# Performance work log

Hardware: AMD Instinct MI355X
Metric: run time of the kernel (lower is better)

## Reference

```python
import jax, jax.numpy as jnp
import numpy as np

N_NODES = 100000


def gcn_conv(x, edge_index, W, b, n_nodes):
    """PyG GCNConv: h = x @ W; add self-loops; symmetric deg norm; sum-aggregate; + bias."""
    src, dst = edge_index[0], edge_index[1]
    loop = jnp.arange(n_nodes, dtype=src.dtype)
    src = jnp.concatenate([src, loop])  # [E + N]
    dst = jnp.concatenate([dst, loop])
    w = jnp.ones(src.shape[0], dtype=x.dtype)  # edge_weight=None -> ones
    deg = jax.ops.segment_sum(w, dst, num_segments=n_nodes)  # in-degree incl. self-loop
    dinv = jnp.where(deg > 0, jax.lax.rsqrt(deg), 0.0).astype(x.dtype)
    norm = dinv[src] * w * dinv[dst]  # [E + N]
    h = x @ W  # [N, d_out] transform first (PyG order)
    msgs = norm[:, None] * h[src]  # [E + N, d_out] gathered, normalized messages
    out = jax.ops.segment_sum(msgs, dst, num_segments=n_nodes)
    return out + b


def setup_inputs() -> dict:
    key = jax.random.key(0)
    k1, k2, k3, k4 = jax.random.split(key, 4)
    d_in, d_hid, d_out = 128, 128, 64
    E = 3200000
    x = jax.random.normal(k1, (N_NODES, d_in), dtype=jnp.float32)
    edge_index = jax.random.randint(k2, (2, E), 0, N_NODES, dtype=jnp.int64)
    W1 = jax.random.normal(k3, (d_in, d_hid), dtype=jnp.float32) / np.sqrt(d_in)
    b1 = jnp.zeros((d_hid,), dtype=jnp.float32)
    W2 = jax.random.normal(k4, (d_hid, d_out), dtype=jnp.float32) / np.sqrt(d_hid)
    b2 = jnp.zeros((d_out,), dtype=jnp.float32)
    return {"x": x, "edge_index": edge_index, "W1": W1, "b1": b1, "W2": W2, "b2": b2}


def reference(x, edge_index, W1, b1, W2, b2):
    h = gcn_conv(x, edge_index, W1, b1, N_NODES)
    h = jax.nn.relu(h)
    out = gcn_conv(h, edge_index, W2, b2, N_NODES)
    return out
```

## Files before the change

kernel.cpp:

```cpp
#include <hip/hip_runtime.h>


#define N_NODES 100000
#define NBLK2 256
#define NBUCK2 782
#define NCH 13
#define NKEY (NBUCK2 * NCH)

#define FPS  1048576.0f
#define INVS 9.5367431640625e-7f

typedef __attribute__((ext_vector_type(8))) short short8;
typedef __attribute__((ext_vector_type(4))) float f32x4;

__device__ __forceinline__ unsigned short f2bf(float f) {
    union { float f; unsigned u; } c; c.f = f;
    unsigned r = (c.u + 0x7fffu + ((c.u >> 16) & 1u)) >> 16;
    return (unsigned short)r;
}
__device__ __forceinline__ float2 bfpair(unsigned u) {
    union { float f; unsigned u; } a, b;
    a.u = u << 16; b.u = u & 0xffff0000u;
    return make_float2(a.f, b.f);
}
__device__ __forceinline__ unsigned packbf(float a, float b) {
    return (unsigned)f2bf(a) | ((unsigned)f2bf(b) << 16);
}
__device__ __forceinline__ int fp20(float v) {
    return __float2int_rn(v * FPS);
}

__global__ void detect64_k(const unsigned long long* __restrict__ ei, int* __restrict__ flag) {
    unsigned long long v = ei[threadIdx.x & 63];
    unsigned long long bad = __ballot(v >= (1ULL << 32));
    if (threadIdx.x == 0) *flag = (bad == 0ULL) ? 1 : 0;
}

__device__ __forceinline__ int edge_at(const void* ei, int is64, long long idx) {
    if (is64) return (int)((const long long*)ei)[idx];
    return ((const int*)ei)[idx];
}

__global__ __launch_bounds__(256) void count1_k(const void* __restrict__ ei,
                                                const int* __restrict__ flag,
                                                int* __restrict__ bhist, int E) {
    __shared__ int lh[NKEY];
    int t = threadIdx.x;
    for (int i = t; i < NKEY; i += 256) lh[i] = 0;
    __syncthreads();
    int is64 = *flag;
    int C = (E + NBLK2 - 1) / NBLK2;
    int lo = blockIdx.x * C;
    int hi = lo + C; if (hi > E) hi = E;
    for (int e = lo + t; e < hi; e += 256) {
        int s = edge_at(ei, is64, e);
        int d = edge_at(ei, is64, (long long)E + e);
        if ((unsigned)d >= (unsigned)N_NODES) continue;
        if ((unsigned)s >= (unsigned)N_NODES) s = 0;
        atomicAdd(&lh[(d >> 7) * NCH + (s >> 13)], 1);
    }
    __syncthreads();
    int* dst = bhist + (size_t)blockIdx.x * NKEY;
    for (int i = t; i < NKEY; i += 256) dst[i] = lh[i];
}

__global__ void colsum_k(const int* __restrict__ bhist, int* __restrict__ colsum) {
    int k = blockIdx.x * 256 + threadIdx.x;
    if (k >= NKEY) return;
    int s = 0;
#pragma unroll 4
    for (int b = 0; b < NBLK2; ++b) s += bhist[(size_t)b * NKEY + k];
    colsum[k] = s;
}

__global__ void scan1_k(const int* __restrict__ cnt, int* __restrict__ partial,
                        int* __restrict__ bsum, int n) {
    __shared__ int sm[256];
    int t = threadIdx.x;
    int base = blockIdx.x * 1024 + t * 4;
    int v[4]; int loc = 0;
#pragma unroll
    for (int j = 0; j < 4; ++j) { v[j] = (base + j < n) ? cnt[base + j] : 0; loc += v[j]; }
    sm[t] = loc; __syncthreads();
    for (int off = 1; off < 256; off <<= 1) {
        int x = (t >= off) ? sm[t - off] : 0;
        __syncthreads();
        sm[t] += x;
        __syncthreads();
    }
    int incl = sm[t];
    int run = incl - loc;
    if (t == 255) bsum[blockIdx.x] = incl;
#pragma unroll
    for (int j = 0; j < 4; ++j) {
        if (base + j < n) partial[base + j] = run;
        run += v[j];
    }
}

__global__ void scan2_k(int* __restrict__ bsum, int nb) {
    __shared__ int sm[256];
    int t = threadIdx.x;
    int v[16]; int loc = 0;
#pragma unroll
    for (int i = 0; i < 16; ++i) {
        int idx = t * 16 + i;
        v[i] = (idx < nb) ? bsum[idx] : 0;
        loc += v[i];
    }
    sm[t] = loc; __syncthreads();
    for (int off = 1; off < 256; off <<= 1) {
        int x = (t >= off) ? sm[t - off] : 0;
        __syncthreads();
        sm[t] += x;
        __syncthreads();
    }
    int run = sm[t] - loc;
#pragma unroll
    for (int i = 0; i < 16; ++i) {
        int idx = t * 16 + i;
        if (idx < nb) bsum[idx] = run;
        run += v[i];
    }
}

__global__ void scanadd_k(const int* __restrict__ bsum, int* __restrict__ arr,
                          const int* __restrict__ raw, int* __restrict__ tot, int n) {
    int base = blockIdx.x * 1024 + threadIdx.x * 4;
    int add = bsum[blockIdx.x];
#pragma unroll
    for (int j = 0; j < 4; ++j) {
        int i = base + j;
        if (i < n) {
            int v = arr[i] + add;
            arr[i] = v;
            if (i == n - 1) *tot = v + raw[i];
        }
    }
}

__global__ void colprefix_k(const int* __restrict__ bhist, const int* __restrict__ keybase,
                            int* __restrict__ bbase) {
    int k = blockIdx.x * 256 + threadIdx.x;
    if (k >= NKEY) return;
    int run = keybase[k];
#pragma unroll 8
    for (int b = 0; b < NBLK2; ++b) {
        size_t i = (size_t)b * NKEY + k;
        int c = bhist[i];
        bbase[i] = run;
        run += c;
    }
}

__global__ void dinv_k(const int* __restrict__ cnt, float* __restrict__ dinv, int n) {
    int i = blockIdx.x * 256 + threadIdx.x;
    if (i < n) dinv[i] = rsqrtf((float)(cnt[i] + 1));
}

__global__ __launch_bounds__(256) void write1_k(const void* __restrict__ ei,
                                                const int* __restrict__ flag,
                                                const int* __restrict__ bbase,
                                                unsigned* __restrict__ pairs, int E) {
    __shared__ int lofs[NKEY];
    int t = threadIdx.x;
    const int* src0 = bbase + (size_t)blockIdx.x * NKEY;
    for (int i = t; i < NKEY; i += 256) lofs[i] = src0[i];
    __syncthreads();
    int is64 = *flag;
    int C = (E + NBLK2 - 1) / NBLK2;
    int lo = blockIdx.x * C;
    int hi = lo + C; if (hi > E) hi = E;
    for (int e = lo + t; e < hi; e += 256) {
        int s = edge_at(ei, is64, e);
        int d = edge_at(ei, is64, (long long)E + e);
        if ((unsigned)d >= (unsigned)N_NODES) continue;
        if ((unsigned)s >= (unsigned)N_NODES) s = 0;
        int key = (d >> 7) * NCH + (s >> 13);
        int p = atomicAdd(&lofs[key], 1);
        pairs[p] = (unsigned)s | ((unsigned)(d & 127) << 17);
    }
}

__global__ __launch_bounds__(256) void degree_k(const unsigned* __restrict__ pairs,
                                                const int* __restrict__ keybase,
                                                const int* __restrict__ tot,
                                                int* __restrict__ cnt, int Nn) {
    __shared__ int lh[128];
    int b = blockIdx.x;
    int t = threadIdx.x;
    if (t < 128) lh[t] = 0;
    __syncthreads();
    int lo = keybase[b * NCH];
    int hi = (b == NBUCK2 - 1) ? *tot : keybase[(b + 1) * NCH];
    for (int i = lo + t; i < hi; i += 256) {
        unsigned p = __builtin_nontemporal_load(pairs + i);
        atomicAdd(&lh[p >> 17], 1);
    }
    __syncthreads();
    int n0 = b << 7;
    if (t < 128 && n0 + t < Nn) cnt[n0 + t] = lh[t];
}

__global__ void prep_w_k(const float* __restrict__ W1, const float* __restrict__ W2,
                         unsigned short* __restrict__ w1bf, unsigned short* __restrict__ w2bf) {
    int i = blockIdx.x * 256 + threadIdx.x;
    if (i < 128 * 128) { int k = i >> 7, f = i & 127; w1bf[f * 128 + k] = f2bf(W1[i]); }
    if (i < 128 * 64)  { int k = i >> 6, f = i & 63;  w2bf[f * 128 + k] = f2bf(W2[i]); }
}

__global__ __launch_bounds__(256) void gemm1_k(const float* __restrict__ x,
                                               const unsigned short* __restrict__ w1bf,
                                               const float* __restrict__ dinv,
                                               unsigned* __restrict__ h1, int Nn) {
    __shared__ __align__(16) unsigned short sA[128][136];
    __shared__ __align__(16) unsigned short sB[64][136];
    int tid = threadIdx.x;
    int n0g = blockIdx.x * 64;
    {
        const uint4* src = (const uint4*)w1bf;
#pragma unroll
        for (int l = 0; l < 8; ++l) {
            int idx = tid + l * 256;
            int f = idx >> 4, kq = idx & 15;
            *(uint4*)&sA[f][kq * 8] = src[idx];
        }
    }
    {
        int n = tid >> 2, kq = tid & 3;
        int gn = n0g + n; if (gn >= Nn) gn = Nn - 1;
        const float4* xr = (const float4*)(x + (size_t)gn * 128 + kq * 32);
        unsigned short* dst = &sB[n][kq * 32];
#pragma unroll
        for (int i = 0; i < 8; ++i) {
            float4 v = xr[i];
            dst[i * 4 + 0] = f2bf(v.x); dst[i * 4 + 1] = f2bf(v.y);
            dst[i * 4 + 2] = f2bf(v.z); dst[i * 4 + 3] = f2bf(v.w);
        }
    }
    __syncthreads();
    int wave = tid >> 6, lane = tid & 63;
    int quad = lane >> 4, l16 = lane & 15;
    f32x4 z = {0.f, 0.f, 0.f, 0.f};
    f32x4 acc[8];
#pragma unroll
    for (int t = 0; t < 8; ++t) acc[t] = z;
#pragma unroll
    for (int kk = 0; kk < 4; ++kk) {
        int kb = kk * 32 + quad * 8;
        short8 a = *(const short8*)&sB[wave * 16 + l16][kb];
#pragma unroll
        for (int ft = 0; ft < 8; ++ft) {
            short8 b = *(const short8*)&sA[ft * 16 + l16][kb];
            acc[ft] = __builtin_amdgcn_mfma_f32_16x16x32_bf16(a, b, acc[ft], 0, 0, 0);
        }
    }
    float dv[4];
#pragma unroll
    for (int r = 0; r < 4; ++r) {
        int gn = n0g + wave * 16 + quad * 4 + r;
        if (gn >= Nn) gn = Nn - 1;
        dv[r] = dinv[gn];
    }
    __syncthreads();
    unsigned short (*sC)[136] = sA;
#pragma unroll
    for (int ft = 0; ft < 8; ++ft)
#pragma unroll
        for (int r = 0; r < 4; ++r)
            sC[wave * 16 + quad * 4 + r][ft * 16 + l16] = f2bf(dv[r] * acc[ft][r]);
    __syncthreads();
#pragma unroll
    for (int l = 0; l < 4; ++l) {
        int idx = tid + l * 256;
        int row = idx >> 4, g = idx & 15;
        int gn = n0g + row;
        if (gn < Nn) {
            ushort4 A = *(ushort4*)&sC[row][g * 4];
            ushort4 B = *(ushort4*)&sC[row][g * 4 + 64];
            uint4 o;
            o.x = (unsigned)A.x | ((unsigned)B.x << 16);
            o.y = (unsigned)A.y | ((unsigned)B.y << 16);
            o.z = (unsigned)A.z | ((unsigned)B.z << 16);
            o.w = (unsigned)A.w | ((unsigned)B.w << 16);
            *(uint4*)&h1[(size_t)gn * 64 + g * 4] = o;
        }
    }
}

__global__ __launch_bounds__(256) void gemm2_k(const unsigned* __restrict__ hr,
                                               const unsigned short* __restrict__ w2bf,
                                               const float* __restrict__ dinv,
                                               unsigned* __restrict__ h2, int Nn) {
    __shared__ __align__(16) unsigned short sA[64][136];
    __shared__ __align__(16) unsigned short sB[64][136];
    int tid = threadIdx.x;
    int n0g = blockIdx.x * 64;
    {
        const uint4* src = (const uint4*)w2bf;
#pragma unroll
        for (int l = 0; l < 4; ++l) {
            int idx = tid + l * 256;
            int f = idx >> 4, kq = idx & 15;
            *(uint4*)&sA[f][kq * 8] = src[idx];
        }
    }
    {
        const uint4* src = (const uint4*)hr;
#pragma unroll
        for (int l = 0; l < 4; ++l) {
            int idx = tid + l * 256;
            int row = idx >> 4, q = idx & 15;
            int gn = n0g + row; if (gn >= Nn) gn = Nn - 1;
            *(uint4*)&sB[row][q * 8] = src[(size_t)gn * 16 + q];
        }
    }
    __syncthreads();
    int wave = tid >> 6, lane = tid & 63;
    int quad = lane >> 4, l16 = lane & 15;
    f32x4 z = {0.f, 0.f, 0.f, 0.f};
    f32x4 acc[4];
#pragma unroll
    for (int t = 0; t < 4; ++t) acc[t] = z;
#pragma unroll
    for (int kk = 0; kk < 4; ++kk) {
        int kb = kk * 32 + quad * 8;
        short8 a = *(const short8*)&sB[wave * 16 + l16][kb];
#pragma unroll
        for (int ft = 0; ft < 4; ++ft) {
            short8 b = *(const short8*)&sA[ft * 16 + l16][kb];
            acc[ft] = __builtin_amdgcn_mfma_f32_16x16x32_bf16(a, b, acc[ft], 0, 0, 0);
        }
    }
    float dv[4];
#pragma unroll
    for (int r = 0; r < 4; ++r) {
        int gn = n0g + wave * 16 + quad * 4 + r;
        if (gn >= Nn) gn = Nn - 1;
        dv[r] = dinv[gn];
    }
    __syncthreads();
    unsigned short (*sC)[136] = sA;
#pragma unroll
    for (int ft = 0; ft < 4; ++ft)
#pragma unroll
        for (int r = 0; r < 4; ++r)
            sC[wave * 16 + quad * 4 + r][ft * 16 + l16] = f2bf(dv[r] * acc[ft][r]);
    __syncthreads();
#pragma unroll
    for (int l = 0; l < 2; ++l) {
        int idx = tid + l * 256;
        int row = idx >> 3, g = idx & 7;
        int gn = n0g + row;
        if (gn < Nn) {
            ushort4 A = *(ushort4*)&sC[row][g * 4];
            ushort4 B = *(ushort4*)&sC[row][g * 4 + 32];
            uint4 o;
            o.x = (unsigned)A.x | ((unsigned)B.x << 16);
            o.y = (unsigned)A.y | ((unsigned)B.y << 16);
            o.z = (unsigned)A.z | ((unsigned)B.z << 16);
            o.w = (unsigned)A.w | ((unsigned)B.w << 16);
            *(uint4*)&h2[(size_t)gn * 32 + g * 4] = o;
        }
    }
}

__global__ __launch_bounds__(512) void agg1_k(const unsigned* __restrict__ h,
                                              const unsigned* __restrict__ pairs,
                                              const int* __restrict__ keybase,
                                              const int* __restrict__ tot,
                                              const float* __restrict__ dinv,
                                              const float* __restrict__ bias,
                                              unsigned* __restrict__ out, int Nn) {
    extern __shared__ int iacc[];
    int tid = threadIdx.x, lane = tid & 63, wave = tid >> 6;
    int b = blockIdx.x, n0 = b << 7;
    for (int i = tid; i < 128 * 64; i += 512) {
        int row = i >> 6, q = i & 63;
        unsigned u = (n0 + row < Nn) ? h[(size_t)(n0 + row) * 64 + q] : 0u;
        float2 v = bfpair(u);
        iacc[row * 128 + q] = fp20(v.x);
        iacc[row * 128 + 64 + q] = fp20(v.y);
    }
    __syncthreads();
    int lo = keybase[b * NCH];
    int hi = (b == NBUCK2 - 1) ? *tot : keybase[(b + 1) * NCH];
    for (int base = lo + wave * 64; base < hi; base += 512) {
        int idx = base + lane;
        unsigned pv = pairs[(idx < hi) ? idx : (hi - 1)];
        int m = hi - base; if (m > 64) m = 64;
        int j = 0;
        for (; j + 4 <= m; j += 4) {
            unsigned p0 = __shfl(pv, j),     p1 = __shfl(pv, j + 1);
            unsigned p2 = __shfl(pv, j + 2), p3 = __shfl(pv, j + 3);
            unsigned u0 = h[((p0 & 0x1FFFFu) << 6) + lane];
            unsigned u1 = h[((p1 & 0x1FFFFu) << 6) + lane];
            unsigned u2 = h[((p2 & 0x1FFFFu) << 6) + lane];
            unsigned u3 = h[((p3 & 0x1FFFFu) << 6) + lane];
            float2 v0 = bfpair(u0); int* a0 = &iacc[((p0 >> 17) << 7) + lane];
            atomicAdd(a0, fp20(v0.x)); atomicAdd(a0 + 64, fp20(v0.y));
            float2 v1 = bfpair(u1); int* a1 = &iacc[((p1 >> 17) << 7) + lane];
            atomicAdd(a1, fp20(v1.x)); atomicAdd(a1 + 64, fp20(v1.y));
            float2 v2 = bfpair(u2); int* a2 = &iacc[((p2 >> 17) << 7) + lane];
            atomicAdd(a2, fp20(v2.x)); atomicAdd(a2 + 64, fp20(v2.y));
            float2 v3 = bfpair(u3); int* a3 = &iacc[((p3 >> 17) << 7) + lane];
            atomicAdd(a3, fp20(v3.x)); atomicAdd(a3 + 64, fp20(v3.y));
        }
        for (; j < m; ++j) {
            unsigned p = __shfl(pv, j);
            unsigned u = h[((p & 0x1FFFFu) << 6) + lane];
            float2 v = bfpair(u);
            int* a = &iacc[((p >> 17) << 7) + lane];
            atomicAdd(a, fp20(v.x)); atomicAdd(a + 64, fp20(v.y));
        }
    }
    __syncthreads();
    int nn = Nn - n0; if (nn > 128) nn = 128;
    for (int i = tid; i < nn * 64; i += 512) {
        int row = i >> 6, q = i & 63;
        float di = dinv[n0 + row];
        float sx = (float)iacc[row * 128 + 2 * q] * INVS;
        float sy = (float)iacc[row * 128 + 2 * q + 1] * INVS;
        float r0 = fmaxf(fmaf(di, sx, bias[2 * q]), 0.f);
        float r1 = fmaxf(fmaf(di, sy, bias[2 * q + 1]), 0.f);
        out[(size_t)(n0 + row) * 64 + q] = packbf(r0, r1);
    }
}

__global__ __launch_bounds__(512) void agg2_k(const unsigned* __restrict__ h,
                                              const unsigned* __restrict__ pairs,
                                              const int* __restrict__ keybase,
                                              const int* __restrict__ tot,
                                              const float* __restrict__ dinv,
                                              const float* __restrict__ bias,
                                              float* __restrict__ out, int Nn) {
    __shared__ int iacc[128 * 64];
    int tid = threadIdx.x, lane = tid & 63, wave = tid >> 6;
    int half = lane >> 5, fl = lane & 31;
    int b = blockIdx.x, n0 = b << 7;
    for (int i = tid; i < 128 * 32; i += 512) {
        int row = i >> 5, q = i & 31;
        unsigned u = (n0 + row < Nn) ? h[(size_t)(n0 + row) * 32 + q] : 0u;
        float2 v = bfpair(u);
        iacc[row * 64 + q] = fp20(v.x);
        iacc[row * 64 + 32 + q] = fp20(v.y);
    }
    __syncthreads();
    int lo = keybase[b * NCH];
    int hi = (b == NBUCK2 - 1) ? *tot : keybase[(b + 1) * NCH];
    for (int base = lo + wave * 64; base < hi; base += 512) {
        int idx = base + lane;
        unsigned pv = pairs[(idx < hi) ? idx : (hi - 1)];
        int m = hi - base; if (m > 64) m = 64;
        int j = 0;
        for (; j + 8 <= m; j += 8) {
            unsigned p0 = __shfl(pv, j + half);
            unsigned p1 = __shfl(pv, j + 2 + half);
            unsigned p2 = __shfl(pv, j + 4 + half);
            unsigned p3 = __shfl(pv, j + 6 + half);
            unsigned u0 = h[((p0 & 0x1FFFFu) << 5) + fl];
            unsigned u1 = h[((p1 & 0x1FFFFu) << 5) + fl];
            unsigned u2 = h[((p2 & 0x1FFFFu) << 5) + fl];
            unsigned u3 = h[((p3 & 0x1FFFFu) << 5) + fl];
            float2 v0 = bfpair(u0); int* a0 = &iacc[((p0 >> 17) << 6) + fl];
            atomicAdd(a0, fp20(v0.x)); atomicAdd(a0 + 32, fp20(v0.y));
            float2 v1 = bfpair(u1); int* a1 = &iacc[((p1 >> 17) << 6) + fl];
            atomicAdd(a1, fp20(v1.x)); atomicAdd(a1 + 32, fp20(v1.y));
            float2 v2 = bfpair(u2); int* a2 = &iacc[((p2 >> 17) << 6) + fl];
            atomicAdd(a2, fp20(v2.x)); atomicAdd(a2 + 32, fp20(v2.y));
            float2 v3 = bfpair(u3); int* a3 = &iacc[((p3 >> 17) << 6) + fl];
            atomicAdd(a3, fp20(v3.x)); atomicAdd(a3 + 32, fp20(v3.y));
        }
        for (; j < m; j += 2) {
            int q = j + half;
            unsigned p = __shfl(pv, (q < m) ? q : j);
            if (q < m) {
                unsigned u = h[((p & 0x1FFFFu) << 5) + fl];
                float2 v = bfpair(u);
                int* a = &iacc[((p >> 17) << 6) + fl];
                atomicAdd(a, fp20(v.x)); atomicAdd(a + 32, fp20(v.y));
            }
        }
    }
    __syncthreads();
    int nn = Nn - n0; if (nn > 128) nn = 128;
    for (int i = tid; i < nn * 64; i += 512) {
        int row = i >> 6, f = i & 63;
        float di = dinv[n0 + row];
        float s = (float)iacc[row * 64 + f] * INVS;
        out[(size_t)(n0 + row) * 64 + f] = fmaf(di, s, bias[f]);
    }
}

extern "C" void kernel_launch(void* const* d_in, const int* in_sizes, int n_in,
                              void* d_out, int out_size, void* d_ws, size_t ws_size,
                              hipStream_t stream) {
    const float* x  = (const float*)d_in[0];
    const void*  ei = d_in[1];
    const float* W1 = (const float*)d_in[2];
    const float* b1 = (const float*)d_in[3];
    const float* W2 = (const float*)d_in[4];
    const float* b2 = (const float*)d_in[5];

    const int N = N_NODES;
    const int E = in_sizes[1] / 2;

    char* w = (char*)d_ws;
    size_t off = 0;
    auto take = [&](size_t bytes) {
        void* p = w + off;
        off = (off + bytes + 255) & ~(size_t)255;
        return p;
    };
    int*   flag    = (int*)take(2 * sizeof(int));
    int*   tot     = flag + 1;
    int*   cnt     = (int*)take((size_t)N * 4);
    int*   bsumB   = (int*)take(4096 * 4);
    int*   colsum  = (int*)take((size_t)NKEY * 4);
    int*   keybase = (int*)take((size_t)NKEY * 4);
    float* dinv    = (float*)take((size_t)N * 4);
    unsigned* pairs = (unsigned*)take((size_t)E * 4);
    unsigned short* w1bf = (unsigned short*)take(128 * 128 * 2);
    unsigned short* w2bf = (unsigned short*)take(64 * 128 * 2);
    unsigned* hr   = (unsigned*)take((size_t)N * 64 * 4);
    unsigned* h2   = (unsigned*)take((size_t)N * 32 * 4);
    (void)ws_size; (void)n_in; (void)out_size;

    int* bhist = (int*)hr;
    int* bbase = (int*)h2;

    unsigned* h1 = (unsigned*)d_out;

    const int nscanK = (NKEY + 1023) / 1024;
    const int ngridK = (NKEY + 255) / 256;

    detect64_k<<<1, 64, 0, stream>>>((const unsigned long long*)ei, flag);
    count1_k<<<NBLK2, 256, 0, stream>>>(ei, flag, bhist, E);
    colsum_k<<<ngridK, 256, 0, stream>>>(bhist, colsum);
    scan1_k<<<nscanK, 256, 0, stream>>>(colsum, keybase, bsumB, NKEY);
    scan2_k<<<1, 256, 0, stream>>>(bsumB, nscanK);
    scanadd_k<<<nscanK, 256, 0, stream>>>(bsumB, keybase, colsum, tot, NKEY);
    colprefix_k<<<ngridK, 256, 0, stream>>>(bhist, keybase, bbase);
    write1_k<<<NBLK2, 256, 0, stream>>>(ei, flag, bbase, pairs, E);
    degree_k<<<NBUCK2, 256, 0, stream>>>(pairs, keybase, tot, cnt, N);
    dinv_k<<<(N + 255) / 256, 256, 0, stream>>>(cnt, dinv, N);
    prep_w_k<<<64, 256, 0, stream>>>(W1, W2, w1bf, w2bf);

    gemm1_k<<<(N + 63) / 64, 256, 0, stream>>>(x, w1bf, dinv, h1, N);
    agg1_k<<<NBUCK2, 512, 128 * 128 * 4, stream>>>(h1, pairs, keybase, tot, dinv, b1, hr, N);
    gemm2_k<<<(N + 63) / 64, 256, 0, stream>>>(hr, w2bf, dinv, h2, N);
    agg2_k<<<NBUCK2, 512, 0, stream>>>(h2, pairs, keybase, tot, dinv, b2, (float*)d_out, N);
}
```

Baseline: 484.6 us.

## Store GEMM outputs as int16 fixed-point and widen aggregation blocks to 1024 threads

```diff
diff --git a/kernel.cpp b/kernel.cpp
--- a/kernel.cpp
+++ b/kernel.cpp
@@ -7,8 +7,8 @@
 #define NCH 13
 #define NKEY (NBUCK2 * NCH)
 
-#define FPS  1048576.0f
-#define INVS 9.5367431640625e-7f
+#define QS   8192.0f
+#define IQS  1.220703125e-4f
 
 typedef __attribute__((ext_vector_type(8))) short short8;
 typedef __attribute__((ext_vector_type(4))) float f32x4;
@@ -18,16 +18,13 @@
     unsigned r = (c.u + 0x7fffu + ((c.u >> 16) & 1u)) >> 16;
     return (unsigned short)r;
 }
-__device__ __forceinline__ float2 bfpair(unsigned u) {
-    union { float f; unsigned u; } a, b;
-    a.u = u << 16; b.u = u & 0xffff0000u;
-    return make_float2(a.f, b.f);
-}
 __device__ __forceinline__ unsigned packbf(float a, float b) {
     return (unsigned)f2bf(a) | ((unsigned)f2bf(b) << 16);
 }
-__device__ __forceinline__ int fp20(float v) {
-    return __float2int_rn(v * FPS);
+__device__ __forceinline__ unsigned short q13(float v) {
+    int i = __float2int_rn(v * QS);
+    i = i < -32767 ? -32767 : (i > 32767 ? 32767 : i);
+    return (unsigned short)(i & 0xffff);
 }
 
 __global__ void detect64_k(const unsigned long long* __restrict__ ei, int* __restrict__ flag) {
@@ -268,7 +265,7 @@
     for (int ft = 0; ft < 8; ++ft)
 #pragma unroll
         for (int r = 0; r < 4; ++r)
-            sC[wave * 16 + quad * 4 + r][ft * 16 + l16] = f2bf(dv[r] * acc[ft][r]);
+            sC[wave * 16 + quad * 4 + r][ft * 16 + l16] = q13(dv[r] * acc[ft][r]);
     __syncthreads();
 #pragma unroll
     for (int l = 0; l < 4; ++l) {
@@ -345,7 +342,7 @@
     for (int ft = 0; ft < 4; ++ft)
 #pragma unroll
         for (int r = 0; r < 4; ++r)
-            sC[wave * 16 + quad * 4 + r][ft * 16 + l16] = f2bf(dv[r] * acc[ft][r]);
+            sC[wave * 16 + quad * 4 + r][ft * 16 + l16] = q13(dv[r] * acc[ft][r]);
     __syncthreads();
 #pragma unroll
     for (int l = 0; l < 2; ++l) {
@@ -365,27 +362,26 @@
     }
 }
 
-__global__ __launch_bounds__(512) void agg1_k(const unsigned* __restrict__ h,
-                                              const unsigned* __restrict__ pairs,
-                                              const int* __restrict__ keybase,
-                                              const int* __restrict__ tot,
-                                              const float* __restrict__ dinv,
-                                              const float* __restrict__ bias,
-                                              unsigned* __restrict__ out, int Nn) {
+__global__ __launch_bounds__(1024) void agg1_k(const unsigned* __restrict__ h,
+                                               const unsigned* __restrict__ pairs,
+                                               const int* __restrict__ keybase,
+                                               const int* __restrict__ tot,
+                                               const float* __restrict__ dinv,
+                                               const float* __restrict__ bias,
+                                               unsigned* __restrict__ out, int Nn) {
     extern __shared__ int iacc[];
     int tid = threadIdx.x, lane = tid & 63, wave = tid >> 6;
     int b = blockIdx.x, n0 = b << 7;
-    for (int i = tid; i < 128 * 64; i += 512) {
+    for (int i = tid; i < 128 * 64; i += 1024) {
         int row = i >> 6, q = i & 63;
         unsigned u = (n0 + row < Nn) ? h[(size_t)(n0 + row) * 64 + q] : 0u;
-        float2 v = bfpair(u);
-        iacc[row * 128 + q] = fp20(v.x);
-        iacc[row * 128 + 64 + q] = fp20(v.y);
+        iacc[row * 128 + q] = (int)(short)(u & 0xffffu);
+        iacc[row * 128 + 64 + q] = ((int)u) >> 16;
     }
     __syncthreads();
     int lo = keybase[b * NCH];
     int hi = (b == NBUCK2 - 1) ? *tot : keybase[(b + 1) * NCH];
-    for (int base = lo + wave * 64; base < hi; base += 512) {
+    for (int base = lo + wave * 64; base < hi; base += 1024) {
         int idx = base + lane;
         unsigned pv = pairs[(idx < hi) ? idx : (hi - 1)];
         int m = hi - base; if (m > 64) m = 64;
@@ -397,58 +393,56 @@
             unsigned u1 = h[((p1 & 0x1FFFFu) << 6) + lane];
             unsigned u2 = h[((p2 & 0x1FFFFu) << 6) + lane];
             unsigned u3 = h[((p3 & 0x1FFFFu) << 6) + lane];
-            float2 v0 = bfpair(u0); int* a0 = &iacc[((p0 >> 17) << 7) + lane];
-            atomicAdd(a0, fp20(v0.x)); atomicAdd(a0 + 64, fp20(v0.y));
-            float2 v1 = bfpair(u1); int* a1 = &iacc[((p1 >> 17) << 7) + lane];
-            atomicAdd(a1, fp20(v1.x)); atomicAdd(a1 + 64, fp20(v1.y));
-            float2 v2 = bfpair(u2); int* a2 = &iacc[((p2 >> 17) << 7) + lane];
-            atomicAdd(a2, fp20(v2.x)); atomicAdd(a2 + 64, fp20(v2.y));
-            float2 v3 = bfpair(u3); int* a3 = &iacc[((p3 >> 17) << 7) + lane];
-            atomicAdd(a3, fp20(v3.x)); atomicAdd(a3 + 64, fp20(v3.y));
+            int* a0 = &iacc[((p0 >> 17) << 7) + lane];
+            atomicAdd(a0, (int)(short)(u0 & 0xffffu)); atomicAdd(a0 + 64, ((int)u0) >> 16);
+            int* a1 = &iacc[((p1 >> 17) << 7) + lane];
+            atomicAdd(a1, (int)(short)(u1 & 0xffffu)); atomicAdd(a1 + 64, ((int)u1) >> 16);
+            int* a2 = &iacc[((p2 >> 17) << 7) + lane];
+            atomicAdd(a2, (int)(short)(u2 & 0xffffu)); atomicAdd(a2 + 64, ((int)u2) >> 16);
+            int* a3 = &iacc[((p3 >> 17) << 7) + lane];
+            atomicAdd(a3, (int)(short)(u3 & 0xffffu)); atomicAdd(a3 + 64, ((int)u3) >> 16);
         }
         for (; j < m; ++j) {
             unsigned p = __shfl(pv, j);
             unsigned u = h[((p & 0x1FFFFu) << 6) + lane];
-            float2 v = bfpair(u);
             int* a = &iacc[((p >> 17) << 7) + lane];
-            atomicAdd(a, fp20(v.x)); atomicAdd(a + 64, fp20(v.y));
+            atomicAdd(a, (int)(short)(u & 0xffffu)); atomicAdd(a + 64, ((int)u) >> 16);
         }
     }
     __syncthreads();
     int nn = Nn - n0; if (nn > 128) nn = 128;
-    for (int i = tid; i < nn * 64; i += 512) {
+    for (int i = tid; i < nn * 64; i += 1024) {
         int row = i >> 6, q = i & 63;
         float di = dinv[n0 + row];
-        float sx = (float)iacc[row * 128 + 2 * q] * INVS;
-        float sy = (float)iacc[row * 128 + 2 * q + 1] * INVS;
+        float sx = (float)iacc[row * 128 + 2 * q] * IQS;
+        float sy = (float)iacc[row * 128 + 2 * q + 1] * IQS;
         float r0 = fmaxf(fmaf(di, sx, bias[2 * q]), 0.f);
         float r1 = fmaxf(fmaf(di, sy, bias[2 * q + 1]), 0.f);
         out[(size_t)(n0 + row) * 64 + q] = packbf(r0, r1);
     }
 }
 
-__global__ __launch_bounds__(512) void agg2_k(const unsigned* __restrict__ h,
-                                              const unsigned* __restrict__ pairs,
-                                              const int* __restrict__ keybase,
-                                              const int* __restrict__ tot,
-                                              const float* __restrict__ dinv,
-                                              const float* __restrict__ bias,
-                                              float* __restrict__ out, int Nn) {
+__global__ __launch_bounds__(1024) void agg2_k(const unsigned* __restrict__ h,
+                                               const unsigned* __restrict__ pairs,
+                                               const int* __restrict__ keybase,
+                                               const int* __restrict__ tot,
+                                               const float* __restrict__ dinv,
+                                               const float* __restrict__ bias,
+                                               float* __restrict__ out, int Nn) {
     __shared__ int iacc[128 * 64];
     int tid = threadIdx.x, lane = tid & 63, wave = tid >> 6;
     int half = lane >> 5, fl = lane & 31;
     int b = blockIdx.x, n0 = b << 7;
-    for (int i = tid; i < 128 * 32; i += 512) {
+    for (int i = tid; i < 128 * 32; i += 1024) {
         int row = i >> 5, q = i & 31;
         unsigned u = (n0 + row < Nn) ? h[(size_t)(n0 + row) * 32 + q] : 0u;
-        float2 v = bfpair(u);
-        iacc[row * 64 + q] = fp20(v.x);
-        iacc[row * 64 + 32 + q] = fp20(v.y);
+        iacc[row * 64 + q] = (int)(short)(u & 0xffffu);
+        iacc[row * 64 + 32 + q] = ((int)u) >> 16;
     }
     __syncthreads();
     int lo = keybase[b * NCH];
     int hi = (b == NBUCK2 - 1) ? *tot : keybase[(b + 1) * NCH];
-    for (int base = lo + wave * 64; base < hi; base += 512) {
+    for (int base = lo + wave * 64; base < hi; base += 1024) {
         int idx = base + lane;
         unsigned pv = pairs[(idx < hi) ? idx : (hi - 1)];
         int m = hi - base; if (m > 64) m = 64;
@@ -462,32 +456,31 @@
             unsigned u1 = h[((p1 & 0x1FFFFu) << 5) + fl];
             unsigned u2 = h[((p2 & 0x1FFFFu) << 5) + fl];
             unsigned u3 = h[((p3 & 0x1FFFFu) << 5) + fl];
-            float2 v0 = bfpair(u0); int* a0 = &iacc[((p0 >> 17) << 6) + fl];
-            atomicAdd(a0, fp20(v0.x)); atomicAdd(a0 + 32, fp20(v0.y));
-            float2 v1 = bfpair(u1); int* a1 = &iacc[((p1 >> 17) << 6) + fl];
-            atomicAdd(a1, fp20(v1.x)); atomicAdd(a1 + 32, fp20(v1.y));
-            float2 v2 = bfpair(u2); int* a2 = &iacc[((p2 >> 17) << 6) + fl];
-            atomicAdd(a2, fp20(v2.x)); atomicAdd(a2 + 32, fp20(v2.y));
-            float2 v3 = bfpair(u3); int* a3 = &iacc[((p3 >> 17) << 6) + fl];
-            atomicAdd(a3, fp20(v3.x)); atomicAdd(a3 + 32, fp20(v3.y));
+            int* a0 = &iacc[((p0 >> 17) << 6) + fl];
+            atomicAdd(a0, (int)(short)(u0 & 0xffffu)); atomicAdd(a0 + 32, ((int)u0) >> 16);
+            int* a1 = &iacc[((p1 >> 17) << 6) + fl];
+            atomicAdd(a1, (int)(short)(u1 & 0xffffu)); atomicAdd(a1 + 32, ((int)u1) >> 16);
+            int* a2 = &iacc[((p2 >> 17) << 6) + fl];
+            atomicAdd(a2, (int)(short)(u2 & 0xffffu)); atomicAdd(a2 + 32, ((int)u2) >> 16);
+            int* a3 = &iacc[((p3 >> 17) << 6) + fl];
+            atomicAdd(a3, (int)(short)(u3 & 0xffffu)); atomicAdd(a3 + 32, ((int)u3) >> 16);
         }
         for (; j < m; j += 2) {
             int q = j + half;
             unsigned p = __shfl(pv, (q < m) ? q : j);
             if (q < m) {
                 unsigned u = h[((p & 0x1FFFFu) << 5) + fl];
-                float2 v = bfpair(u);
                 int* a = &iacc[((p >> 17) << 6) + fl];
-                atomicAdd(a, fp20(v.x)); atomicAdd(a + 32, fp20(v.y));
+                atomicAdd(a, (int)(short)(u & 0xffffu)); atomicAdd(a + 32, ((int)u) >> 16);
             }
         }
     }
     __syncthreads();
     int nn = Nn - n0; if (nn > 128) nn = 128;
-    for (int i = tid; i < nn * 64; i += 512) {
+    for (int i = tid; i < nn * 64; i += 1024) {
         int row = i >> 6, f = i & 63;
         float di = dinv[n0 + row];
-        float s = (float)iacc[row * 64 + f] * INVS;
+        float s = (float)iacc[row * 64 + f] * IQS;
         out[(size_t)(n0 + row) * 64 + f] = fmaf(di, s, bias[f]);
     }
 }
@@ -547,7 +540,7 @@
     prep_w_k<<<64, 256, 0, stream>>>(W1, W2, w1bf, w2bf);
 
     gemm1_k<<<(N + 63) / 64, 256, 0, stream>>>(x, w1bf, dinv, h1, N);
-    agg1_k<<<NBUCK2, 512, 128 * 128 * 4, stream>>>(h1, pairs, keybase, tot, dinv, b1, hr, N);
+    agg1_k<<<NBUCK2, 1024, 128 * 128 * 4, stream>>>(h1, pairs, keybase, tot, dinv, b1, hr, N);
     gemm2_k<<<(N + 63) / 64, 256, 0, stream>>>(hr, w2bf, dinv, h2, N);
-    agg2_k<<<NBUCK2, 512, 0, stream>>>(h2, pairs, keybase, tot, dinv, b2, (float*)d_out, N);
-}
+    agg2_k<<<NBUCK2, 1024, 0, stream>>>(h2, pairs, keybase, tot, dinv, b2, (float*)d_out, N);
+}
```

After: 441.1 us. 1.1x faster.
